# Kernel tuning notes

Measured on AMD Instinct MI355X. Metric: run time of the kernel, lower is better.

## Reference

```python
import jax, jax.numpy as jnp
import numpy as np

N_NODES = 50000
N_EDGES = 800000
DIM = 64
BN_EPS = 1e-5


def setup_inputs() -> dict:
    key = jax.random.key(0)
    ks = jax.random.split(key, 9)
    s = 1.0 / np.sqrt(DIM)
    feature = jax.random.normal(ks[0], (N_NODES, DIM), jnp.float32)
    edge_index = jax.random.randint(ks[1], (2, N_EDGES), 0, N_NODES)
    Wk = jax.random.normal(ks[2], (DIM, DIM), jnp.float32) * s
    Wq = jax.random.normal(ks[3], (DIM, DIM), jnp.float32) * s
    Wv = jax.random.normal(ks[4], (DIM, DIM), jnp.float32) * s
    bk = jax.random.normal(ks[5], (DIM,), jnp.float32) * 0.01
    bq = jax.random.normal(ks[6], (DIM,), jnp.float32) * 0.01
    bv = jax.random.normal(ks[7], (DIM,), jnp.float32) * 0.01
    bias = jax.random.normal(ks[8], (DIM,), jnp.float32) * 0.01
    gamma = jnp.ones((DIM,), jnp.float32)
    beta = jnp.zeros((DIM,), jnp.float32)
    return dict(feature=feature, edge_index=edge_index, Wk=Wk, bk=bk,
                Wq=Wq, bq=bq, Wv=Wv, bv=bv, bias=bias, gamma=gamma, beta=beta)


def reference(feature, edge_index, Wk, bk, Wq, bq, Wv, bv, bias, gamma, beta):
    # Node-level projections (dense GEMMs on [N, D])
    K = feature @ Wk + bk   # applied to x_i (dst)
    Q = feature @ Wq + bq   # applied to x_j (src)
    V = feature @ Wv + bv   # applied to x_j (src)
    src, dst = edge_index[0], edge_index[1]
    # Per-edge gather -> sigmoid gate -> gated message  [E, D]
    eta = jax.nn.sigmoid(K[dst] + Q[src])
    msg = eta * V[src]
    # Scatter-add into destination nodes  [N, D]
    agg = jax.ops.segment_sum(msg, dst, num_segments=feature.shape[0])
    h = agg + bias
    # BatchNorm1d over nodes (batch statistics, biased variance) + ReLU
    mean = jnp.mean(h, axis=0)
    var = jnp.var(h, axis=0)
    h = (h - mean) * jax.lax.rsqrt(var + BN_EPS) * gamma + beta
    return jax.nn.relu(h)
```

## Files before the change

### kernel.cpp

```cpp
#include <hip/hip_runtime.h>
#include <hip/hip_fp16.h>
#include <stdint.h>

#define N_NODES 50000
#define N_EDGES 800000
#define DIM 64
#define BN_EPS 1e-5f
#define CAP 64
#define ZERO_NODE N_NODES
#define POISON 0xAAAAAAAAu

#define NPTILES 391
#define FUSED_BLOCKS 1173

#define NTILES 3125
#define NSTATS_REP 8

typedef _Float16 f16;
typedef __attribute__((ext_vector_type(8))) _Float16 f16x8;
typedef __attribute__((ext_vector_type(4))) float f32x4;

__global__ __launch_bounds__(256, 4) void proj_scatter_kernel(
    const float* __restrict__ feat,
    const float* __restrict__ Wk, const float* __restrict__ Wq,
    const float* __restrict__ Wv,
    const float* __restrict__ bk, const float* __restrict__ bq,
    const float* __restrict__ bv,
    __half* __restrict__ Kh, __half* __restrict__ QV,
    const int* __restrict__ ei, uint32_t* __restrict__ counts,
    uint16_t* __restrict__ bucket)
{
  const int b = blockIdx.x;
  const int tid = threadIdx.x;
  const int m3 = b % 3;

  if (m3 != 0) {
    const int sid = (b / 3) * 2 + (m3 - 1);
    const int e0 = sid * 1024;
    const int e1 = (e0 + 1024 < N_EDGES) ? e0 + 1024 : N_EDGES;
    const int base = e0 + tid * 4;
    if (base >= e1) return;
    if (base + 4 <= e1) {
      const int4 s4 = *(const int4*)(ei + base);
      const int4 d4 = *(const int4*)(ei + N_EDGES + base);
      const int ss[4] = {s4.x, s4.y, s4.z, s4.w};
      const int dd[4] = {d4.x, d4.y, d4.z, d4.w};
      uint32_t pos[4];
#pragma unroll
      for (int i = 0; i < 4; ++i)
        pos[i] = atomicAdd(&counts[dd[i]], 1u) - POISON;
#pragma unroll
      for (int i = 0; i < 4; ++i)
        if (pos[i] < CAP) bucket[(size_t)dd[i] * CAP + pos[i]] = (uint16_t)ss[i];
    } else {
      for (int e = base; e < e1; ++e) {
        const int src = ei[e];
        const int dst = ei[N_EDGES + e];
        const uint32_t pos = atomicAdd(&counts[dst], 1u) - POISON;
        if (pos < CAP) bucket[(size_t)dst * CAP + pos] = (uint16_t)src;
      }
    }
    return;
  }

  const int tile0 = (b / 3) * 128;
  const int lane = tid & 63;
  const int w = tid >> 6;
  const int nl = lane & 15;
  const int kg = lane >> 4;

  f16x8 fb[2][2];
#pragma unroll
  for (int g2 = 0; g2 < 2; ++g2) {
    const int node = tile0 + w * 32 + g2 * 16 + nl;
    const bool ok = node < N_NODES;
    const float* fp = feat + (size_t)(ok ? node : 0) * DIM;
#pragma unroll
    for (int kk = 0; kk < 2; ++kk) {
      const float4 x0 = ((const float4*)(fp + kk * 32 + kg * 8))[0];
      const float4 x1 = ((const float4*)(fp + kk * 32 + kg * 8))[1];
      f16x8 r;
      r[0] = (f16)x0.x; r[1] = (f16)x0.y; r[2] = (f16)x0.z; r[3] = (f16)x0.w;
      r[4] = (f16)x1.x; r[5] = (f16)x1.y; r[6] = (f16)x1.z; r[7] = (f16)x1.w;
      if (!ok) r = (f16x8)(f16)0.f;
      fb[g2][kk] = r;
    }
  }

#pragma unroll
  for (int m = 0; m < 3; ++m) {
    const float* __restrict__ Wm = (m == 0) ? Wk : (m == 1) ? Wq : Wv;
    const float* __restrict__ bb = (m == 0) ? bk : (m == 1) ? bq : bv;

    f16x8 fa[4][2];
#pragma unroll
    for (int nt = 0; nt < 4; ++nt)
#pragma unroll
      for (int kk = 0; kk < 2; ++kk) {
        f16x8 r;
#pragma unroll
        for (int j = 0; j < 8; ++j)
          r[j] = (f16)Wm[(kk * 32 + kg * 8 + j) * 64 + nt * 16 + nl];
        fa[nt][kk] = r;
      }
    f32x4 bias[4];
#pragma unroll
    for (int nt = 0; nt < 4; ++nt)
      bias[nt] = *(const f32x4*)&bb[nt * 16 + kg * 4];

#pragma unroll
    for (int g2 = 0; g2 < 2; ++g2) {
      const int node = tile0 + w * 32 + g2 * 16 + nl;
      f32x4 acc[4];
#pragma unroll
      for (int nt = 0; nt < 4; ++nt) acc[nt] = bias[nt];
#pragma unroll
      for (int kk = 0; kk < 2; ++kk)
#pragma unroll
        for (int nt = 0; nt < 4; ++nt)
          acc[nt] = __builtin_amdgcn_mfma_f32_16x16x32_f16(
              fa[nt][kk], fb[g2][kk], acc[nt], 0, 0, 0);

      if (m == 0) {
        if (node < N_NODES) {
#pragma unroll
          for (int nt = 0; nt < 4; ++nt) {
            union { __half2 h[2]; uint2 u; } pk;
            pk.h[0] = __floats2half2_rn(acc[nt][0], acc[nt][1]);
            pk.h[1] = __floats2half2_rn(acc[nt][2], acc[nt][3]);
            ((uint2*)Kh)[node * 16 + nt * 4 + kg] = pk.u;
          }
        }
      } else {
        if (node <= N_NODES) {
          const int half = (m == 1) ? 0 : 1;
#pragma unroll
          for (int nt = 0; nt < 4; ++nt) {
            union { __half2 h[2]; uint2 u; } pk;
            pk.h[0] = __floats2half2_rn(acc[nt][0], acc[nt][1]);
            pk.h[1] = __floats2half2_rn(acc[nt][2], acc[nt][3]);
            if (node == N_NODES) { pk.u.x = 0u; pk.u.y = 0u; }
            ((uint2*)QV)[node * 32 + (nt * 4 + kg) * 2 + half] = pk.u;
          }
        }
      }
    }
  }
}

__device__ __forceinline__ float4 edge_acc(float4 acc, const float4 k,
                                           const uint4 qv)
{
  union { uint32_t u; __half2 h; } q0, q1, v0, v1;
  q0.u = qv.x; q1.u = qv.y; v0.u = qv.z; v1.u = qv.w;
  const float2 qa = __half22float2(q0.h);
  const float2 qb = __half22float2(q1.h);
  const float2 va = __half22float2(v0.h);
  const float2 vb = __half22float2(v1.h);
  acc.x += va.x * __builtin_amdgcn_rcpf(1.0f + __expf(-(k.x + qa.x)));
  acc.y += va.y * __builtin_amdgcn_rcpf(1.0f + __expf(-(k.y + qa.y)));
  acc.z += vb.x * __builtin_amdgcn_rcpf(1.0f + __expf(-(k.z + qb.x)));
  acc.w += vb.y * __builtin_amdgcn_rcpf(1.0f + __expf(-(k.w + qb.y)));
  return acc;
}

__global__ __launch_bounds__(256) void aggregate_kernel(
    const uint32_t* __restrict__ counts, const uint16_t* __restrict__ bucket,
    const uint2* __restrict__ Kh2, const uint4* __restrict__ QV4,
    float4* __restrict__ agg4, float* __restrict__ stats)
{
  const int tid = threadIdx.x;
  const int row = tid >> 4;
  const int t = tid & 15;
  const int n = blockIdx.x * 16 + row;

  union { uint2 u; __half2 h[2]; } kun;
  kun.u = Kh2[n * 16 + t];
  const float2 k0 = __half22float2(kun.h[0]);
  const float2 k1 = __half22float2(kun.h[1]);
  const float4 k = make_float4(k0.x, k0.y, k1.x, k1.y);

  int deg = (int)(counts[n] - POISON);
  if (deg > CAP) deg = CAP;
  const uint16_t* bp = bucket + (size_t)n * CAP;
  float4 acc = make_float4(0.f, 0.f, 0.f, 0.f);

  for (int j0 = 0; j0 < deg; j0 += 16) {
    const int navail = deg - j0;
    const int s = (t < navail) ? (int)bp[j0 + t] : ZERO_NODE;

    int sA[8]; uint4 qvA[8];
#pragma unroll
    for (int i = 0; i < 8; ++i) sA[i] = __shfl(s, i, 16);
#pragma unroll
    for (int i = 0; i < 8; ++i) qvA[i] = QV4[sA[i] * 16 + t];

    const bool haveB = navail > 8;
    int sB[8]; uint4 qvB[8];
    if (haveB) {
#pragma unroll
      for (int i = 0; i < 8; ++i) sB[i] = __shfl(s, 8 + i, 16);
#pragma unroll
      for (int i = 0; i < 8; ++i) qvB[i] = QV4[sB[i] * 16 + t];
    }

#pragma unroll
    for (int i = 0; i < 8; ++i) acc = edge_acc(acc, k, qvA[i]);
    if (haveB) {
#pragma unroll
      for (int i = 0; i < 8; ++i) acc = edge_acc(acc, k, qvB[i]);
    }
  }
  agg4[n * 16 + t] = acc;

  __shared__ float sred[2][16][DIM + 4];
  float4 pssq;
  pssq.x = acc.x * acc.x; pssq.y = acc.y * acc.y;
  pssq.z = acc.z * acc.z; pssq.w = acc.w * acc.w;
  *(float4*)&sred[0][row][t * 4] = acc;
  *(float4*)&sred[1][row][t * 4] = pssq;
  __syncthreads();
  if (tid < 128) {
    const int s = tid >> 6, c = tid & 63;
    float v = 0.0f;
#pragma unroll
    for (int r = 0; r < 16; ++r) v += sred[s][r][c];
    atomicAdd(&stats[(blockIdx.x & (NSTATS_REP - 1)) * 128 + tid], v);
  }
}

__global__ __launch_bounds__(256) void out_kernel(
    float* __restrict__ out, const float* __restrict__ stats,
    const float* __restrict__ gamma, const float* __restrict__ beta)
{
  __shared__ float sstats[128];
  const int tid = threadIdx.x;
  if (tid < 128) {
    float v = 0.0f;
#pragma unroll
    for (int r = 0; r < NSTATS_REP; ++r) v += stats[r * 128 + tid];
    sstats[tid] = v;
  }
  __syncthreads();

  const int idx = blockIdx.x * 256 + tid;
  if (idx >= N_NODES * (DIM / 4)) return;
  const int t = idx & 15;
  const float4 v = ((const float4*)out)[idx];
  const float invN = 1.0f / (float)N_NODES;
  const float vin[4] = { v.x, v.y, v.z, v.w };
  float o[4];
#pragma unroll
  for (int j = 0; j < 4; ++j) {
    const int c = t * 4 + j;
    const float mean = sstats[c] * invN;
    float var = sstats[DIM + c] * invN - mean * mean;
    var = var < 0.0f ? 0.0f : var;
    const float scale = rsqrtf(var + BN_EPS) * gamma[c];
    const float shift = beta[c] - mean * scale;
    const float x = vin[j] * scale + shift;
    o[j] = x > 0.0f ? x : 0.0f;
  }
  float4 r; r.x = o[0]; r.y = o[1]; r.z = o[2]; r.w = o[3];
  ((float4*)out)[idx] = r;
}

extern "C" void kernel_launch(void* const* d_in, const int* in_sizes, int n_in,
                              void* d_out, int out_size, void* d_ws, size_t ws_size,
                              hipStream_t stream) {
  (void)in_sizes; (void)n_in; (void)out_size; (void)ws_size;
  const float* feat  = (const float*)d_in[0];
  const int*   ei    = (const int*)d_in[1];
  const float* Wk    = (const float*)d_in[2];
  const float* bk    = (const float*)d_in[3];
  const float* Wq    = (const float*)d_in[4];
  const float* bq    = (const float*)d_in[5];
  const float* Wv    = (const float*)d_in[6];
  const float* bv    = (const float*)d_in[7];
  const float* gamma = (const float*)d_in[9];
  const float* beta  = (const float*)d_in[10];

  char* base = (char*)d_ws;
  __half*   Kh     = (__half*)base;
  __half*   QV     = (__half*)(base + 6400000);
  float*    stats  = (float*)(base + 19200256);
  uint32_t* counts = (uint32_t*)(base + 19204352);
  uint16_t* bucket = (uint16_t*)(base + 19404352);

  proj_scatter_kernel<<<FUSED_BLOCKS, 256, 0, stream>>>(
      feat, Wk, Wq, Wv, bk, bq, bv, Kh, QV, ei, counts, bucket);

  aggregate_kernel<<<NTILES, 256, 0, stream>>>(
      counts, bucket, (const uint2*)Kh, (const uint4*)QV, (float4*)d_out,
      stats);

  out_kernel<<<(N_NODES * (DIM / 4) + 255) / 256, 256, 0, stream>>>(
      (float*)d_out, stats, gamma, beta);
}
```

Before: 175.2 us.

## Replace global per-node atomic scatter with two-pass binning and LDS-local counting

The edge scatter no longer does one global atomic per edge on per-node counters. Edges are now first binned into 64 coarse destination bins using shared-memory histograms and one global atomic per bin per block, then a separate 64-block kernel builds the per-node buckets with LDS atomics. The weight matrices are also staged transposed into LDS so the MFMA operands are read as vectors instead of strided scalar global loads. The cost is an extra kernel launch and an intermediate array round-trip through memory, and only 64 blocks do the second pass, which may leave much of the GPU idle.

```diff
diff --git a/kernel.cpp b/kernel.cpp
--- a/kernel.cpp
+++ b/kernel.cpp
@@ -13,6 +13,10 @@
 #define NPTILES 391
 #define FUSED_BLOCKS 1173
 
+#define NBINS 64
+#define BIN_W 784
+#define BINCAP 13824
+
 #define NTILES 3125
 #define NSTATS_REP 8
 
@@ -20,16 +24,22 @@
 typedef __attribute__((ext_vector_type(8))) _Float16 f16x8;
 typedef __attribute__((ext_vector_type(4))) float f32x4;
 
-__global__ __launch_bounds__(256, 4) void proj_scatter_kernel(
+#define LPITCH 72
+
+__global__ __launch_bounds__(256, 4) void proj_bin_kernel(
     const float* __restrict__ feat,
     const float* __restrict__ Wk, const float* __restrict__ Wq,
     const float* __restrict__ Wv,
     const float* __restrict__ bk, const float* __restrict__ bq,
     const float* __restrict__ bv,
     __half* __restrict__ Kh, __half* __restrict__ QV,
-    const int* __restrict__ ei, uint32_t* __restrict__ counts,
-    uint16_t* __restrict__ bucket)
-{
+    const int* __restrict__ ei, uint32_t* __restrict__ binCursor,
+    uint32_t* __restrict__ binArr)
+{
+  __shared__ f16 sWt[DIM][LPITCH];
+  __shared__ uint32_t hist[NBINS];
+  __shared__ uint32_t gbase[NBINS];
+
   const int b = blockIdx.x;
   const int tid = threadIdx.x;
   const int m3 = b % 3;
@@ -38,27 +48,43 @@
     const int sid = (b / 3) * 2 + (m3 - 1);
     const int e0 = sid * 1024;
     const int e1 = (e0 + 1024 < N_EDGES) ? e0 + 1024 : N_EDGES;
+    if (tid < NBINS) hist[tid] = 0;
+    __syncthreads();
+
+    int n = 0; int bn[4]; uint32_t pk[4], rk[4];
     const int base = e0 + tid * 4;
-    if (base >= e1) return;
     if (base + 4 <= e1) {
       const int4 s4 = *(const int4*)(ei + base);
       const int4 d4 = *(const int4*)(ei + N_EDGES + base);
       const int ss[4] = {s4.x, s4.y, s4.z, s4.w};
       const int dd[4] = {d4.x, d4.y, d4.z, d4.w};
-      uint32_t pos[4];
-#pragma unroll
-      for (int i = 0; i < 4; ++i)
-        pos[i] = atomicAdd(&counts[dd[i]], 1u) - POISON;
-#pragma unroll
-      for (int i = 0; i < 4; ++i)
-        if (pos[i] < CAP) bucket[(size_t)dd[i] * CAP + pos[i]] = (uint16_t)ss[i];
+#pragma unroll
+      for (int j = 0; j < 4; ++j) {
+        const int bin = dd[j] / BIN_W;
+        bn[j] = bin;
+        pk[j] = (uint32_t)ss[j] | ((uint32_t)(dd[j] - bin * BIN_W) << 16);
+        rk[j] = atomicAdd(&hist[bin], 1u);
+      }
+      n = 4;
     } else {
       for (int e = base; e < e1; ++e) {
         const int src = ei[e];
         const int dst = ei[N_EDGES + e];
-        const uint32_t pos = atomicAdd(&counts[dst], 1u) - POISON;
-        if (pos < CAP) bucket[(size_t)dst * CAP + pos] = (uint16_t)src;
-      }
+        const int bin = dst / BIN_W;
+        bn[n] = bin;
+        pk[n] = (uint32_t)src | ((uint32_t)(dst - bin * BIN_W) << 16);
+        rk[n] = atomicAdd(&hist[bin], 1u);
+        ++n;
+      }
+    }
+    __syncthreads();
+    if (tid < NBINS)
+      gbase[tid] = hist[tid] ? (atomicAdd(&binCursor[tid * 16], hist[tid])
+                                - POISON) : 0u;
+    __syncthreads();
+    for (int j = 0; j < n; ++j) {
+      const uint32_t pos = gbase[bn[j]] + rk[j];
+      if (pos < BINCAP) binArr[(uint32_t)bn[j] * BINCAP + pos] = pk[j];
     }
     return;
   }
@@ -92,17 +118,25 @@
     const float* __restrict__ Wm = (m == 0) ? Wk : (m == 1) ? Wq : Wv;
     const float* __restrict__ bb = (m == 0) ? bk : (m == 1) ? bq : bv;
 
+    __syncthreads();
+    for (int i = tid; i < 1024; i += 256) {
+      const int c = i & 63;
+      const int kq = i >> 6;
+      union { f16 h[4]; uint2 u; } pkw;
+      pkw.h[0] = (f16)Wm[(kq * 4 + 0) * 64 + c];
+      pkw.h[1] = (f16)Wm[(kq * 4 + 1) * 64 + c];
+      pkw.h[2] = (f16)Wm[(kq * 4 + 2) * 64 + c];
+      pkw.h[3] = (f16)Wm[(kq * 4 + 3) * 64 + c];
+      *(uint2*)&sWt[c][kq * 4] = pkw.u;
+    }
+    __syncthreads();
+
     f16x8 fa[4][2];
 #pragma unroll
     for (int nt = 0; nt < 4; ++nt)
 #pragma unroll
-      for (int kk = 0; kk < 2; ++kk) {
-        f16x8 r;
-#pragma unroll
-        for (int j = 0; j < 8; ++j)
-          r[j] = (f16)Wm[(kk * 32 + kg * 8 + j) * 64 + nt * 16 + nl];
-        fa[nt][kk] = r;
-      }
+      for (int kk = 0; kk < 2; ++kk)
+        fa[nt][kk] = *(const f16x8*)&sWt[nt * 16 + nl][kk * 32 + kg * 8];
     f32x4 bias[4];
 #pragma unroll
     for (int nt = 0; nt < 4; ++nt)
@@ -125,10 +159,10 @@
         if (node < N_NODES) {
 #pragma unroll
           for (int nt = 0; nt < 4; ++nt) {
-            union { __half2 h[2]; uint2 u; } pk;
-            pk.h[0] = __floats2half2_rn(acc[nt][0], acc[nt][1]);
-            pk.h[1] = __floats2half2_rn(acc[nt][2], acc[nt][3]);
-            ((uint2*)Kh)[node * 16 + nt * 4 + kg] = pk.u;
+            union { __half2 h[2]; uint2 u; } pkk;
+            pkk.h[0] = __floats2half2_rn(acc[nt][0], acc[nt][1]);
+            pkk.h[1] = __floats2half2_rn(acc[nt][2], acc[nt][3]);
+            ((uint2*)Kh)[node * 16 + nt * 4 + kg] = pkk.u;
           }
         }
       } else {
@@ -136,15 +170,58 @@
           const int half = (m == 1) ? 0 : 1;
 #pragma unroll
           for (int nt = 0; nt < 4; ++nt) {
-            union { __half2 h[2]; uint2 u; } pk;
-            pk.h[0] = __floats2half2_rn(acc[nt][0], acc[nt][1]);
-            pk.h[1] = __floats2half2_rn(acc[nt][2], acc[nt][3]);
-            if (node == N_NODES) { pk.u.x = 0u; pk.u.y = 0u; }
-            ((uint2*)QV)[node * 32 + (nt * 4 + kg) * 2 + half] = pk.u;
+            union { __half2 h[2]; uint2 u; } pkk;
+            pkk.h[0] = __floats2half2_rn(acc[nt][0], acc[nt][1]);
+            pkk.h[1] = __floats2half2_rn(acc[nt][2], acc[nt][3]);
+            if (node == N_NODES) { pkk.u.x = 0u; pkk.u.y = 0u; }
+            ((uint2*)QV)[node * 32 + (nt * 4 + kg) * 2 + half] = pkk.u;
           }
         }
       }
     }
+  }
+}
+
+__global__ __launch_bounds__(256) void scatter_kernel(
+    const uint32_t* __restrict__ binArr, const uint32_t* __restrict__ binCursor,
+    uint32_t* __restrict__ counts, uint16_t* __restrict__ bucket)
+{
+  __shared__ uint32_t lcnt[BIN_W];
+  const int g = blockIdx.x;
+  const int tid = threadIdx.x;
+  for (int i = tid; i < BIN_W; i += 256) lcnt[i] = 0;
+  __syncthreads();
+
+  uint32_t cnt = binCursor[g * 16] - POISON;
+  if (cnt > BINCAP) cnt = BINCAP;
+  const uint32_t* arr = binArr + (uint32_t)g * BINCAP;
+  const int nbase = g * BIN_W;
+
+  for (uint32_t i = tid * 4; i < cnt; i += 1024) {
+    if (i + 4 <= cnt) {
+      const uint4 p4 = *(const uint4*)(arr + i);
+      const uint32_t ps[4] = {p4.x, p4.y, p4.z, p4.w};
+#pragma unroll
+      for (int j = 0; j < 4; ++j) {
+        const uint32_t dl = ps[j] >> 16;
+        const uint32_t r = atomicAdd(&lcnt[dl], 1u);
+        if (r < CAP)
+          bucket[(size_t)(nbase + dl) * CAP + r] = (uint16_t)(ps[j] & 0xFFFFu);
+      }
+    } else {
+      for (uint32_t e = i; e < cnt; ++e) {
+        const uint32_t p = arr[e];
+        const uint32_t dl = p >> 16;
+        const uint32_t r = atomicAdd(&lcnt[dl], 1u);
+        if (r < CAP)
+          bucket[(size_t)(nbase + dl) * CAP + r] = (uint16_t)(p & 0xFFFFu);
+      }
+    }
+  }
+  __syncthreads();
+  for (int i = tid; i < BIN_W; i += 256) {
+    const int node = nbase + i;
+    if (node < N_NODES) counts[node] = lcnt[i] + POISON;
   }
 }
 
@@ -281,14 +358,18 @@
   const float* beta  = (const float*)d_in[10];
 
   char* base = (char*)d_ws;
-  __half*   Kh     = (__half*)base;
-  __half*   QV     = (__half*)(base + 6400000);
-  float*    stats  = (float*)(base + 19200256);
-  uint32_t* counts = (uint32_t*)(base + 19204352);
-  uint16_t* bucket = (uint16_t*)(base + 19404352);
-
-  proj_scatter_kernel<<<FUSED_BLOCKS, 256, 0, stream>>>(
-      feat, Wk, Wq, Wv, bk, bq, bv, Kh, QV, ei, counts, bucket);
+  __half*   Kh       = (__half*)base;
+  __half*   QV       = (__half*)(base + 6400000);
+  float*    stats    = (float*)(base + 19200256);
+  uint32_t* counts   = (uint32_t*)(base + 19204352);
+  uint16_t* bucket   = (uint16_t*)(base + 19404352);
+  uint32_t* binCursor= (uint32_t*)(base + 25804352);
+  uint32_t* binArr   = (uint32_t*)(base + 25808448);
+
+  proj_bin_kernel<<<FUSED_BLOCKS, 256, 0, stream>>>(
+      feat, Wk, Wq, Wv, bk, bq, bv, Kh, QV, ei, binCursor, binArr);
+
+  scatter_kernel<<<NBINS, 256, 0, stream>>>(binArr, binCursor, counts, bucket);
 
   aggregate_kernel<<<NTILES, 256, 0, stream>>>(
       counts, bucket, (const uint2*)Kh, (const uint4*)QV, (float4*)d_out,
```

Result: faster. 161.4 us (-7.8%).
